# Optimization experiments

Measured on AMD Instinct MI355X. Metric: run time of the kernel, lower is better.

Reference implementation:

```python
import jax, jax.numpy as jnp
import numpy as np


def cmul(a, b):
    # complex multiply on (..., 2) real/imag pairs
    ar, ai = a[..., 0], a[..., 1]
    br, bi = b[..., 0], b[..., 1]
    return jnp.stack([ar * br - ai * bi, ar * bi + ai * br], axis=-1)


def butterfly_apply(x, diag, subdiag, superdiag, k):
    # x: [B, n, 2]; tridiagonal-at-offset-k complex matrix applied to x.
    # diag: [n, 2]; subdiag/superdiag padded to [n, 2], first n-k entries used.
    n = x.shape[-2]
    out = cmul(diag, x)
    out = out.at[..., k:, :].add(cmul(subdiag[: n - k], x[..., : n - k, :]))
    out = out.at[..., : n - k, :].add(cmul(superdiag[: n - k], x[..., k:, :]))
    return out


def block_perm(x, logit, s):
    # Soft block permutation: within each contiguous block of size s,
    # mix identity with even-odd separation (prob p0), then mix each half
    # with its reversal (probs p1, p2). Acts identically on real & imag.
    B, n, _ = x.shape
    p = jax.nn.sigmoid(logit)
    y = x.reshape(B, n // s, s, 2)
    eo = jnp.concatenate([y[:, :, 0::2, :], y[:, :, 1::2, :]], axis=2)
    y = (1 - p[0]) * y + p[0] * eo
    h = s // 2
    first = (1 - p[1]) * y[:, :, :h, :] + p[1] * jnp.flip(y[:, :, :h, :], axis=2)
    second = (1 - p[2]) * y[:, :, h:, :] + p[2] * jnp.flip(y[:, :, h:, :], axis=2)
    return jnp.concatenate([first, second], axis=2).reshape(B, n, 2)


def trifat_forward(x, perm_logits, diags, subdiags, superdiags, bias):
    B, n = x.shape
    depth, m = diags.shape[0], diags.shape[1]
    perm_sizes = [n >> i for i in range(m - 1)][::-1]  # 4, 8, ..., n
    # real_to_complex: zero imaginary part
    xc = jnp.stack([x, jnp.zeros_like(x)], axis=-1)  # [B, n, 2]
    for d in range(depth):
        for j, s in enumerate(perm_sizes):
            xc = block_perm(xc, perm_logits[d, j], s)
        for i in range(m):
            k = n >> (i + 1)  # offsets n/2, n/4, ..., 1
            xc = butterfly_apply(xc, diags[d, i], subdiags[d, i], superdiags[d, i], k)
    return xc[..., 0] + bias  # take real part, add bias


def setup_inputs() -> dict:
    key = jax.random.key(0)
    ks = jax.random.split(key, 6)
    B, n, depth = 4096, 1024, 2
    m = int(np.log2(n))
    return {
        "x": jax.random.normal(ks[0], (B, n), jnp.float32),
        "perm_logits": jax.random.normal(ks[1], (depth, m - 1, 3), jnp.float32),
        "diags": jax.random.normal(ks[2], (depth, m, n, 2), jnp.float32),
        "subdiags": jax.random.normal(ks[3], (depth, m, n, 2), jnp.float32),
        "superdiags": jax.random.normal(ks[4], (depth, m, n, 2), jnp.float32),
        "bias": jnp.zeros((n,), jnp.float32),
    }


def reference(x, perm_logits, diags, subdiags, superdiags, bias):
    return trifat_forward(x, perm_logits, diags, subdiags, superdiags, bias)
```

## Files before the change

kernel.cpp:

```cpp
#include <hip/hip_runtime.h>

#define N 1024
#define THREADS 256
#define EPT 4

__device__ __forceinline__ float2* run_pipeline(
    float2* bufA, float2* bufB, int tid,
    const float* __restrict__ logits,
    const float* __restrict__ diags,
    const float* __restrict__ subd,
    const float* __restrict__ supd)
{
    float2* src = bufA;
    float2* dst = bufB;

    for (int d = 0; d < 2; ++d) {
        for (int j = 0; j < 9; ++j) {
            const int s = 4 << j;
            const int h = s >> 1;
            const float* lg = logits + (d * 9 + j) * 3;
            const float p0 = 1.0f / (1.0f + expf(-lg[0]));
            const float p1 = 1.0f / (1.0f + expf(-lg[1]));
            const float p2 = 1.0f / (1.0f + expf(-lg[2]));
#pragma unroll
            for (int e = 0; e < EPT; ++e) {
                const int idx = tid + e * THREADS;
                const int base = idx & ~(s - 1);
                const int t = idx & (s - 1);
                const bool lo = (t < h);

                const int eo_t = lo ? (2 * t) : (2 * (t - h) + 1);
                const float2 xt  = src[idx];
                const float2 xeo = src[base + eo_t];
                float2 yt;
                yt.x = xt.x + p0 * (xeo.x - xt.x);
                yt.y = xt.y + p0 * (xeo.y - xt.y);

                const int tm = lo ? (h - 1 - t) : (s + h - 1 - t);
                const float psel = lo ? p1 : p2;
                const int eo_m = (tm < h) ? (2 * tm) : (2 * (tm - h) + 1);
                const float2 xm   = src[base + tm];
                const float2 xmeo = src[base + eo_m];
                float2 ym;
                ym.x = xm.x + p0 * (xmeo.x - xm.x);
                ym.y = xm.y + p0 * (xmeo.y - xm.y);

                float2 o;
                o.x = yt.x + psel * (ym.x - yt.x);
                o.y = yt.y + psel * (ym.y - yt.y);
                dst[idx] = o;
            }
            __syncthreads();
            float2* tmp = src; src = dst; dst = tmp;
        }
        for (int i = 0; i < 10; ++i) {
            const int k = N >> (i + 1);
            const float2* Dg = (const float2*)(diags + (size_t)((d * 10 + i) * N) * 2);
            const float2* Sb = (const float2*)(subd  + (size_t)((d * 10 + i) * N) * 2);
            const float2* Sp = (const float2*)(supd  + (size_t)((d * 10 + i) * N) * 2);
#pragma unroll
            for (int e = 0; e < EPT; ++e) {
                const int idx = tid + e * THREADS;
                const float2 xv = src[idx];
                const float2 dg = Dg[idx];
                float2 o;
                o.x = dg.x * xv.x - dg.y * xv.y;
                o.y = dg.x * xv.y + dg.y * xv.x;
                if (idx >= k) {
                    const float2 xs = src[idx - k];
                    const float2 sb = Sb[idx - k];
                    o.x += sb.x * xs.x - sb.y * xs.y;
                    o.y += sb.x * xs.y + sb.y * xs.x;
                }
                if (idx < N - k) {
                    const float2 xp = src[idx + k];
                    const float2 sp = Sp[idx];
                    o.x += sp.x * xp.x - sp.y * xp.y;
                    o.y += sp.x * xp.y + sp.y * xp.x;
                }
                dst[idx] = o;
            }
            __syncthreads();
            float2* tmp = src; src = dst; dst = tmp;
        }
    }
    return src;
}

__global__ __launch_bounds__(THREADS) void trifat_kernel_impl(
    const float* __restrict__ x,
    const float* __restrict__ logits,
    const float* __restrict__ diags,
    const float* __restrict__ subd,
    const float* __restrict__ supd,
    const float* __restrict__ bias,
    float* __restrict__ out,
    int B)
{
    __shared__ float2 bufA[N];
    __shared__ float2 bufB[N];

    const int row = blockIdx.x;
    const int tid = threadIdx.x;
    if (row >= B) return;

    const float* xr = x + (size_t)row * N;
#pragma unroll
    for (int e = 0; e < EPT; ++e) {
        int idx = tid + e * THREADS;
        bufA[idx] = make_float2(xr[idx], 0.0f);
    }
    __syncthreads();

    float2* res = run_pipeline(bufA, bufB, tid, logits, diags, subd, supd);

    float* orow = out + (size_t)row * N;
#pragma unroll
    for (int e = 0; e < EPT; ++e) {
        int idx = tid + e * THREADS;
        orow[idx] = res[idx].x + bias[idx];
    }
}

__device__ __forceinline__ unsigned short f2bf_rne(float f) {
    unsigned int u = __float_as_uint(f);
    unsigned int r = u + 0x7fffu + ((u >> 16) & 1u);
    return (unsigned short)(r >> 16);
}

#define TBW 512
#define NB_BUILD 512

__global__ __launch_bounds__(TBW) void prep_kernel(
    const float* __restrict__ logits,
    const float* __restrict__ diags,
    const float* __restrict__ subd,
    const float* __restrict__ supd,
    const float* __restrict__ x,
    unsigned short* __restrict__ Bt,
    unsigned short* __restrict__ A2)
{
    __shared__ __align__(16) float2 buf[2][2][N];
    __shared__ float sig[54];

    const int tid = threadIdx.x;

    if (blockIdx.x >= NB_BUILD) {
        const int cb = blockIdx.x - NB_BUILD;
        const size_t base4 = (size_t)cb * 4096;
#pragma unroll
        for (int r = 0; r < 8; ++r) {
            const size_t g4 = base4 + r * 512 + tid;
            const float4 v = *(const float4*)(x + g4 * 4);
            ushort4 o;
            o.x = f2bf_rne(v.x);
            o.y = f2bf_rne(v.y);
            o.z = f2bf_rne(v.z);
            o.w = f2bf_rne(v.w);
            *(ushort4*)(A2 + g4 * 4) = o;
        }
        return;
    }

    if (blockIdx.x & 256) {
        unsigned long long t0 = __builtin_amdgcn_s_memrealtime();
        while (__builtin_amdgcn_s_memrealtime() - t0 < 64ULL) { }
    }

    const int j0 = blockIdx.x * 2;
    const int t = tid;

#pragma unroll
    for (int b = 0; b < 2; ++b)
#pragma unroll
        for (int v = 0; v < 2; ++v)
#pragma unroll
            for (int e = 0; e < 2; ++e)
                buf[b][v][tid + e * TBW] = make_float2(0.0f, 0.0f);
    if (tid < 54) sig[tid] = 1.0f / (1.0f + __expf(-logits[tid]));
    __syncthreads();
    if (tid < 2) buf[0][tid][j0 + tid] = make_float2(1.0f, 0.0f);
    __syncthreads();

    int sb = 0;
    for (int d = 0; d < 2; ++d) {
        for (int jp = 0; jp < 9; ++jp) {
            const int s = 4 << jp;
            const int h = s >> 1;
            const int hh = s >> 2;
            const float p0 = sig[(d * 9 + jp) * 3 + 0];
            const float p1 = sig[(d * 9 + jp) * 3 + 1];
            const float p2 = sig[(d * 9 + jp) * 3 + 2];

            auto permTask = [&](int wt, int base) {
                int tt, tm;
                float psel;
                if (wt < hh) { tt = wt;              tm = h - 1 - wt;  psel = p1; }
                else         { const int u = wt - hh; tt = h + u; tm = s - 1 - u; psel = p2; }

                const int eot = (tt < h) ? (2 * tt) : (2 * (tt - h) + 1);
                const int eom = (tm < h) ? (2 * tm) : (2 * (tm - h) + 1);

#pragma unroll
                for (int v = 0; v < 2; ++v) {
                    const float2* src = buf[sb][v];
                    float2* dst = buf[sb ^ 1][v];

                    const float2 xt = src[base + tt], xet = src[base + eot];
                    const float2 xm = src[base + tm], xem = src[base + eom];
                    float2 yt, ym;
                    yt.x = xt.x + p0 * (xet.x - xt.x);
                    yt.y = xt.y + p0 * (xet.y - xt.y);
                    ym.x = xm.x + p0 * (xem.x - xm.x);
                    ym.y = xm.y + p0 * (xem.y - xm.y);

                    float2 ot, om;
                    ot.x = yt.x + psel * (ym.x - yt.x);
                    ot.y = yt.y + psel * (ym.y - yt.y);
                    om.x = ym.x + psel * (yt.x - ym.x);
                    om.y = ym.y + psel * (yt.y - ym.y);
                    dst[base + tt] = ot;
                    dst[base + tm] = om;
                }
            };

            if (jp <= 5) {
                const int wv = tid >> 6;
                const int lane = tid & 63;
                if (d == 0) {
                    if (wv == (j0 >> 7) && lane < h) {
                        permTask(lane, (j0 >> (jp + 2)) << (jp + 2));
                    }
                } else {
                    permTask(lane & (h - 1),
                             128 * wv + ((lane >> (jp + 1)) << (jp + 2)));
                }
                asm volatile("s_waitcnt lgkmcnt(0)" ::: "memory");
                sb ^= 1;
            } else {
                if (jp == 6) __syncthreads();

                int w = -1, base = 0;
                if (d == 0) {
                    if (tid < h) {
                        w = tid;
                        base = (j0 >> (jp + 2)) << (jp + 2);
                    }
                } else {
                    w = tid & (h - 1);
                    base = (tid >> (jp + 1)) << (jp + 2);
                }
                if (w >= 0) permTask(w, base);
                __syncthreads();
                sb ^= 1;
            }
        }

        float4 dg4, sb4, sp4;
        {
            const float4* Dg4 = (const float4*)(diags + (size_t)((d * 10) * N) * 2);
            const float4* Sb4 = (const float4*)(subd  + (size_t)((d * 10) * N) * 2);
            const float4* Sp4 = (const float4*)(supd  + (size_t)((d * 10) * N) * 2);
            dg4 = Dg4[t];
            sb4 = (t >= 256) ? Sb4[t - 256] : make_float4(0.f, 0.f, 0.f, 0.f);
            sp4 = (t < 256)  ? Sp4[t]       : make_float4(0.f, 0.f, 0.f, 0.f);
        }
        for (int i = 0; i < 9; ++i) {
            const int k = N >> (i + 1);
            const int k2 = k >> 1;

            float4 dg4n, sb4n, sp4n;
            if (i < 8) {
                const int kn2 = k2 >> 1;
                const float4* Dg4 = (const float4*)(diags + (size_t)((d * 10 + i + 1) * N) * 2);
                const float4* Sb4 = (const float4*)(subd  + (size_t)((d * 10 + i + 1) * N) * 2);
                const float4* Sp4 = (const float4*)(supd  + (size_t)((d * 10 + i + 1) * N) * 2);
                dg4n = Dg4[t];
                sb4n = (t >= kn2)       ? Sb4[t - kn2] : make_float4(0.f, 0.f, 0.f, 0.f);
                sp4n = (t < 512 - kn2)  ? Sp4[t]       : make_float4(0.f, 0.f, 0.f, 0.f);
            }

            const bool has_sb = (t >= k2);
            const bool has_sp = (t < 512 - k2);
#pragma unroll
            for (int v = 0; v < 2; ++v) {
                const float2* src = buf[sb][v];
                const float4 xv = *(const float4*)(&src[2 * t]);
                float4 o;
                o.x = dg4.x * xv.x - dg4.y * xv.y;
                o.y = dg4.x * xv.y + dg4.y * xv.x;
                o.z = dg4.z * xv.z - dg4.w * xv.w;
                o.w = dg4.z * xv.w + dg4.w * xv.z;
                if (has_sb) {
                    const float4 xs = *(const float4*)(&src[2 * t - k]);
                    o.x += sb4.x * xs.x - sb4.y * xs.y;
                    o.y += sb4.x * xs.y + sb4.y * xs.x;
                    o.z += sb4.z * xs.z - sb4.w * xs.w;
                    o.w += sb4.z * xs.w + sb4.w * xs.z;
                }
                if (has_sp) {
                    const float4 xp = *(const float4*)(&src[2 * t + k]);
                    o.x += sp4.x * xp.x - sp4.y * xp.y;
                    o.y += sp4.x * xp.y + sp4.y * xp.x;
                    o.z += sp4.z * xp.z - sp4.w * xp.w;
                    o.w += sp4.z * xp.w + sp4.w * xp.z;
                }
                *(float4*)(&buf[sb ^ 1][v][2 * t]) = o;
            }
            __syncthreads();
            sb ^= 1;
            if (i < 8) { dg4 = dg4n; sb4 = sb4n; sp4 = sp4n; }
        }
        {
            const float2* Dg = (const float2*)(diags + (size_t)((d * 10 + 9) * N) * 2);
            const float2* Sb = (const float2*)(subd  + (size_t)((d * 10 + 9) * N) * 2);
            const float2* Sp = (const float2*)(supd  + (size_t)((d * 10 + 9) * N) * 2);
            const int i0 = 2 * t, i1 = 2 * t + 1;
            const float2 dg0 = Dg[i0], dg1 = Dg[i1];
            const float2 sb0 = (t >= 1) ? Sb[i0 - 1] : make_float2(0.f, 0.f);
            const float2 sb1 = Sb[i0];
            const float2 sp0 = Sp[i0];
            const float2 sp1 = (t < 511) ? Sp[i1] : make_float2(0.f, 0.f);
#pragma unroll
            for (int v = 0; v < 2; ++v) {
                const float2* src = buf[sb][v];
                const float2 x0 = src[i0], x1 = src[i1];
                float2 o0, o1;
                o0.x = dg0.x * x0.x - dg0.y * x0.y;
                o0.y = dg0.x * x0.y + dg0.y * x0.x;
                o1.x = dg1.x * x1.x - dg1.y * x1.y;
                o1.y = dg1.x * x1.y + dg1.y * x1.x;
                if (t >= 1) {
                    const float2 xs = src[i0 - 1];
                    o0.x += sb0.x * xs.x - sb0.y * xs.y;
                    o0.y += sb0.x * xs.y + sb0.y * xs.x;
                }
                o1.x += sb1.x * x0.x - sb1.y * x0.y;
                o1.y += sb1.x * x0.y + sb1.y * x0.x;
                o0.x += sp0.x * x1.x - sp0.y * x1.y;
                o0.y += sp0.x * x1.y + sp0.y * x1.x;
                if (t < 511) {
                    const float2 xp = src[i1 + 1];
                    o1.x += sp1.x * xp.x - sp1.y * xp.y;
                    o1.y += sp1.x * xp.y + sp1.y * xp.x;
                }
                float4 ow;
                ow.x = o0.x; ow.y = o0.y; ow.z = o1.x; ow.w = o1.y;
                *(float4*)(&buf[sb ^ 1][v][i0]) = ow;
            }
            __syncthreads();
            sb ^= 1;
        }
    }

#pragma unroll
    for (int v = 0; v < 2; ++v)
#pragma unroll
        for (int e = 0; e < 2; ++e) {
            const int idx = tid + e * TBW;
            Bt[(size_t)idx * N + (j0 + v)] = f2bf_rne(buf[sb][v][idx].x);
        }
}

typedef __attribute__((ext_vector_type(8))) __bf16 bf16x8;
typedef __attribute__((ext_vector_type(4))) float f32x4;

#define GLB(p) ((const __attribute__((address_space(1))) void*)(p))
#define LDS(p) ((__attribute__((address_space(3))) void*)(p))

__global__ __launch_bounds__(THREADS) void gemm_bf16(
    const unsigned short* __restrict__ A2,
    const unsigned short* __restrict__ Bt,
    const float* __restrict__ bias,
    float* __restrict__ out)
{
    __shared__ __align__(16) unsigned short As[128 * 64];
    __shared__ __align__(16) unsigned short Bs[64 * 64];

    const int m0 = blockIdx.x * 128;
    const int n0 = blockIdx.y * 64;
    const int tid = threadIdx.x;
    const int wave = tid >> 6, lane = tid & 63;
    const int wm = (wave >> 1) * 64, wn = (wave & 1) * 32;
    const int lrow = lane & 15, q = lane >> 4;
    const int r7 = lrow & 7;

    f32x4 acc[4][2] = {};

    for (int kt = 0; kt < 16; ++kt) {
        const int k0 = kt * 64;
        __syncthreads();
        {
            const unsigned short* gA = A2 + (size_t)m0 * N + k0;
            const unsigned short* gB = Bt + (size_t)n0 * N + k0;
#pragma unroll
            for (int r = 0; r < 4; ++r) {
                const int s = r * 256 + tid;
                const int row = s >> 3;
                const int gl = (s & 7) ^ (row & 7);
                __builtin_amdgcn_global_load_lds(GLB(gA + (size_t)row * N + gl * 8),
                                                 LDS(As + s * 8), 16, 0, 0);
            }
#pragma unroll
            for (int r = 0; r < 2; ++r) {
                const int s = r * 256 + tid;
                const int row = s >> 3;
                const int gl = (s & 7) ^ (row & 7);
                __builtin_amdgcn_global_load_lds(GLB(gB + (size_t)row * N + gl * 8),
                                                 LDS(Bs + s * 8), 16, 0, 0);
            }
        }
        __syncthreads();

#pragma unroll
        for (int kk = 0; kk < 64; kk += 32) {
            const int pg = ((kk >> 3) + q) ^ r7;
            bf16x8 a[4], b[2];
#pragma unroll
            for (int mi = 0; mi < 4; ++mi)
                a[mi] = *(const bf16x8*)(As + (wm + mi * 16 + lrow) * 64 + pg * 8);
#pragma unroll
            for (int ni = 0; ni < 2; ++ni)
                b[ni] = *(const bf16x8*)(Bs + (wn + ni * 16 + lrow) * 64 + pg * 8);
#pragma unroll
            for (int mi = 0; mi < 4; ++mi)
#pragma unroll
                for (int ni = 0; ni < 2; ++ni)
                    acc[mi][ni] = __builtin_amdgcn_mfma_f32_16x16x32_bf16(
                        a[mi], b[ni], acc[mi][ni], 0, 0, 0);
        }
    }

#pragma unroll
    for (int ni = 0; ni < 2; ++ni) {
        const int col = n0 + wn + ni * 16 + lrow;
        const float bv = bias[col];
#pragma unroll
        for (int mi = 0; mi < 4; ++mi)
#pragma unroll
            for (int r = 0; r < 4; ++r) {
                const int row = m0 + wm + mi * 16 + q * 4 + r;
                out[(size_t)row * N + col] = acc[mi][ni][r] + bv;
            }
    }
}

extern "C" void kernel_launch(void* const* d_in, const int* in_sizes, int n_in,
                              void* d_out, int out_size, void* d_ws, size_t ws_size,
                              hipStream_t stream) {
    const float* x      = (const float*)d_in[0];
    const float* logits = (const float*)d_in[1];
    const float* diags  = (const float*)d_in[2];
    const float* subd   = (const float*)d_in[3];
    const float* supd   = (const float*)d_in[4];
    const float* bias   = (const float*)d_in[5];
    float* out = (float*)d_out;

    const int B = in_sizes[0] / N;

    const size_t off_Bt = 0;
    const size_t off_A2 = 2u * 1024 * 1024;
    const size_t need   = off_A2 + (size_t)B * N * 2;

    if (ws_size >= need && B == 4096) {
        unsigned short* Bt = (unsigned short*)((char*)d_ws + off_Bt);
        unsigned short* A2 = (unsigned short*)((char*)d_ws + off_A2);

        prep_kernel<<<dim3(NB_BUILD + 256), dim3(TBW), 0, stream>>>(
            logits, diags, subd, supd, x, Bt, A2);
        gemm_bf16<<<dim3(B / 128, 16), dim3(THREADS), 0, stream>>>(A2, Bt, bias, out);
    } else {
        trifat_kernel_impl<<<dim3(B), dim3(THREADS), 0, stream>>>(
            x, logits, diags, subd, supd, bias, out, B);
    }
}
```

Measured before the change: 121.3 us.

## Fuse pairs of butterfly stages to halve shared-memory barriers in prep kernel

Butterfly stages 0-7 are now processed in pairs. Each thread recomputes the intermediate stage outputs it needs (its own plus two neighbours at offset k/2) straight from the source buffer, then applies the second stage, so each pair needs one __syncthreads and one buffer round trip instead of two. The cost is about three times the first-stage arithmetic, extra shared and global parameter loads, and the loss of the register prefetch of the next stage's coefficients. Stage 8 keeps its own pass.

```diff
diff --git a/kernel.cpp b/kernel.cpp
--- a/kernel.cpp
+++ b/kernel.cpp
@@ -128,6 +128,13 @@
     return (unsigned short)(r >> 16);
 }
 
+__device__ __forceinline__ void cmac4(float4& o, const float4 c, const float4 x) {
+    o.x += c.x * x.x - c.y * x.y;
+    o.y += c.x * x.y + c.y * x.x;
+    o.z += c.z * x.z - c.w * x.w;
+    o.w += c.z * x.w + c.w * x.z;
+}
+
 #define TBW 512
 #define NB_BUILD 512
 
@@ -256,32 +263,66 @@
             }
         }
 
-        float4 dg4, sb4, sp4;
+        for (int m = 0; m < 4; ++m) {
+            const int iA = d * 10 + 2 * m;
+            const int k1 = N >> (2 * m + 1);
+            const int GA = k1 >> 1;
+            const int GB = k1 >> 2;
+            const float4* DgA = (const float4*)(diags + (size_t)(iA * N) * 2);
+            const float4* SbA = (const float4*)(subd  + (size_t)(iA * N) * 2);
+            const float4* SpA = (const float4*)(supd  + (size_t)(iA * N) * 2);
+            const float4* DgB = (const float4*)(diags + (size_t)((iA + 1) * N) * 2);
+            const float4* SbB = (const float4*)(subd  + (size_t)((iA + 1) * N) * 2);
+            const float4* SpB = (const float4*)(supd  + (size_t)((iA + 1) * N) * 2);
+
+#pragma unroll
+            for (int v = 0; v < 2; ++v) {
+                const float2* srcv = buf[sb][v];
+
+                auto u4 = [&](int gq) -> float4 {
+                    const float4 xv = *(const float4*)(&srcv[2 * gq]);
+                    const float4 dA = DgA[gq];
+                    float4 u;
+                    u.x = dA.x * xv.x - dA.y * xv.y;
+                    u.y = dA.x * xv.y + dA.y * xv.x;
+                    u.z = dA.z * xv.z - dA.w * xv.w;
+                    u.w = dA.z * xv.w + dA.w * xv.z;
+                    if (gq >= GA) {
+                        const float4 xs = *(const float4*)(&srcv[2 * (gq - GA)]);
+                        cmac4(u, SbA[gq - GA], xs);
+                    }
+                    if (gq < 512 - GA) {
+                        const float4 xp = *(const float4*)(&srcv[2 * (gq + GA)]);
+                        cmac4(u, SpA[gq], xp);
+                    }
+                    return u;
+                };
+
+                const float4 uc = u4(t);
+                const float4 dB = DgB[t];
+                float4 y;
+                y.x = dB.x * uc.x - dB.y * uc.y;
+                y.y = dB.x * uc.y + dB.y * uc.x;
+                y.z = dB.z * uc.z - dB.w * uc.w;
+                y.w = dB.z * uc.w + dB.w * uc.z;
+                if (t >= GB)       cmac4(y, SbB[t - GB], u4(t - GB));
+                if (t < 512 - GB)  cmac4(y, SpB[t],      u4(t + GB));
+                *(float4*)(&buf[sb ^ 1][v][2 * t]) = y;
+            }
+            __syncthreads();
+            sb ^= 1;
+        }
+
         {
-            const float4* Dg4 = (const float4*)(diags + (size_t)((d * 10) * N) * 2);
-            const float4* Sb4 = (const float4*)(subd  + (size_t)((d * 10) * N) * 2);
-            const float4* Sp4 = (const float4*)(supd  + (size_t)((d * 10) * N) * 2);
-            dg4 = Dg4[t];
-            sb4 = (t >= 256) ? Sb4[t - 256] : make_float4(0.f, 0.f, 0.f, 0.f);
-            sp4 = (t < 256)  ? Sp4[t]       : make_float4(0.f, 0.f, 0.f, 0.f);
-        }
-        for (int i = 0; i < 9; ++i) {
-            const int k = N >> (i + 1);
-            const int k2 = k >> 1;
-
-            float4 dg4n, sb4n, sp4n;
-            if (i < 8) {
-                const int kn2 = k2 >> 1;
-                const float4* Dg4 = (const float4*)(diags + (size_t)((d * 10 + i + 1) * N) * 2);
-                const float4* Sb4 = (const float4*)(subd  + (size_t)((d * 10 + i + 1) * N) * 2);
-                const float4* Sp4 = (const float4*)(supd  + (size_t)((d * 10 + i + 1) * N) * 2);
-                dg4n = Dg4[t];
-                sb4n = (t >= kn2)       ? Sb4[t - kn2] : make_float4(0.f, 0.f, 0.f, 0.f);
-                sp4n = (t < 512 - kn2)  ? Sp4[t]       : make_float4(0.f, 0.f, 0.f, 0.f);
-            }
-
-            const bool has_sb = (t >= k2);
-            const bool has_sp = (t < 512 - k2);
+            const int i = d * 10 + 8;
+            const float4* Dg4 = (const float4*)(diags + (size_t)(i * N) * 2);
+            const float4* Sb4 = (const float4*)(subd  + (size_t)(i * N) * 2);
+            const float4* Sp4 = (const float4*)(supd  + (size_t)(i * N) * 2);
+            const bool has_sb = (t >= 1);
+            const bool has_sp = (t < 511);
+            const float4 dg4 = Dg4[t];
+            const float4 sb4 = has_sb ? Sb4[t - 1] : make_float4(0.f, 0.f, 0.f, 0.f);
+            const float4 sp4 = has_sp ? Sp4[t]     : make_float4(0.f, 0.f, 0.f, 0.f);
 #pragma unroll
             for (int v = 0; v < 2; ++v) {
                 const float2* src = buf[sb][v];
@@ -292,25 +333,19 @@
                 o.z = dg4.z * xv.z - dg4.w * xv.w;
                 o.w = dg4.z * xv.w + dg4.w * xv.z;
                 if (has_sb) {
-                    const float4 xs = *(const float4*)(&src[2 * t - k]);
-                    o.x += sb4.x * xs.x - sb4.y * xs.y;
-                    o.y += sb4.x * xs.y + sb4.y * xs.x;
-                    o.z += sb4.z * xs.z - sb4.w * xs.w;
-                    o.w += sb4.z * xs.w + sb4.w * xs.z;
+                    const float4 xs = *(const float4*)(&src[2 * t - 2]);
+                    cmac4(o, sb4, xs);
                 }
                 if (has_sp) {
-                    const float4 xp = *(const float4*)(&src[2 * t + k]);
-                    o.x += sp4.x * xp.x - sp4.y * xp.y;
-                    o.y += sp4.x * xp.y + sp4.y * xp.x;
-                    o.z += sp4.z * xp.z - sp4.w * xp.w;
-                    o.w += sp4.z * xp.w + sp4.w * xp.z;
+                    const float4 xp = *(const float4*)(&src[2 * t + 2]);
+                    cmac4(o, sp4, xp);
                 }
                 *(float4*)(&buf[sb ^ 1][v][2 * t]) = o;
             }
             __syncthreads();
             sb ^= 1;
-            if (i < 8) { dg4 = dg4n; sb4 = sb4n; sp4 = sp4n; }
-        }
+        }
+
         {
             const float2* Dg = (const float2*)(diags + (size_t)((d * 10 + 9) * N) * 2);
             const float2* Sb = (const float2*)(subd  + (size_t)((d * 10 + 9) * N) * 2);
```

New measurement: 159.2 us. +31.2%, slower.
